# Performance work log

Measured on AMD Instinct MI355X. Metric: run time of the kernel, lower is better.

Reference implementation:

```python
import jax, jax.numpy as jnp
import numpy as np
from jax import lax

FPLANE = 256
RATIO = 0.5
C_SHIFT = int(FPLANE * RATIO)  # 128
HALF = C_SHIFT // 2            # 64


def setup_inputs() -> dict:
    key = jax.random.key(0)
    k_x, k_wl, k_bl, k_wr, k_br = jax.random.split(key, 5)
    T, C, H, W = 64, FPLANE, 56, 56
    x = jax.random.normal(k_x, (T, C, H, W), dtype=jnp.float32)
    # Conv3d(HALF -> 1, kernel (3,3,3)); original inits to zero, we use small
    # random weights so the gated path is non-trivial for kernel testing.
    scale = 1.0 / np.sqrt(HALF * 27)
    w_l = jax.random.normal(k_wl, (1, HALF, 3, 3, 3), dtype=jnp.float32) * scale
    b_l = jax.random.normal(k_bl, (1,), dtype=jnp.float32) * 0.01
    w_r = jax.random.normal(k_wr, (1, HALF, 3, 3, 3), dtype=jnp.float32) * scale
    b_r = jax.random.normal(k_br, (1,), dtype=jnp.float32) * 0.01
    return {"x": x, "w_l": w_l, "b_l": b_l, "w_r": w_r, "b_r": b_r}


def _cyclic_pad_t(x):
    # x: (1, C, T, H, W) -> pad 1 frame cyclically along T
    return jnp.concatenate([x[:, :, -1:], x, x[:, :, :1]], axis=2)


def _conv3d(x, w, b):
    # temporal padding VALID (input is cyclically pre-padded), spatial SAME
    y = lax.conv_general_dilated(
        x, w, window_strides=(1, 1, 1),
        padding=[(0, 0), (1, 1), (1, 1)],
        dimension_numbers=("NCDHW", "OIDHW", "NCDHW"))
    return y + b[None, :, None, None, None]


def reference(x, w_l, b_l, w_r, b_r):
    # x: (T, C, H, W) -> (1, C, T, H, W)
    x5 = x.transpose(1, 0, 2, 3)[None]
    x_l = x5[:, :HALF]                 # (1, half, T, H, W)
    x_r = x5[:, HALF:C_SHIFT]
    x_keep = x5[:, C_SHIFT:]

    gate_l = jnp.tanh(_conv3d(_cyclic_pad_t(x_l), w_l, b_l))  # (1,1,T,H,W)
    gate_r = jnp.tanh(_conv3d(_cyclic_pad_t(x_r), w_r, b_r))

    y_l = gate_l * x_l
    y_r = gate_r * x_r
    y_l = jnp.roll(y_l, -1, axis=2) + (x_l - y_l)
    y_r = jnp.roll(y_r, 1, axis=2) + (x_r - y_r)

    y_all = jnp.concatenate([y_l, y_r, x_keep], axis=1)  # (1, C, T, H, W)
    return y_all[0].transpose(1, 0, 2, 3)                # (T, C, H, W)
```

## Files before the change

kernel.cpp:

```cpp
#include <hip/hip_runtime.h>
#include <math.h>

#define T_DIM 64
#define C_DIM 256
#define H_DIM 56
#define W_DIM 56
#define HW    (H_DIM * W_DIM)
#define HW4   (HW / 4)
#define CHW   (C_DIM * HW)
#define THW   (T_DIM * HW)

typedef float nt_float4 __attribute__((ext_vector_type(4)));

__device__ __forceinline__ float rfl(float v) {
    return __int_as_float(__builtin_amdgcn_readfirstlane(__float_as_int(v)));
}

template<int S>
__global__ __launch_bounds__(256) void gate_kernel(
    const float* __restrict__ x,
    const float* __restrict__ w_l,
    const float* __restrict__ w_r,
    float* __restrict__ pbuf)
{
    constexpr int CPG = 64 / S;

    const int bx   = blockIdx.x;
    const int tq   = bx & 31;
    const int sg   = bx >> 5;
    const int side = sg / S;
    const int g    = sg & (S - 1);

    const int waveid = __builtin_amdgcn_readfirstlane((int)(threadIdx.x >> 6));
    const int hh = waveid & 1;
    const int t  = tq * 2 + (waveid >> 1);

    const int lane = threadIdx.x & 63;
    const int wg   = lane & 15;
    const int rg   = lane >> 4;
    const bool act = (wg < 14);
    const int w0   = act ? wg * 4 : 52;
    const int r0   = hh * 28 + rg * 7;
    const bool have_l = (wg > 0);
    const bool have_r = (wg < 13);

    const float* wtab = (side ? w_r : w_l) + g * CPG * 27;
    const int c0 = side * 64 + g * CPG;

    const int tm = (t + 63) & 63, tp = (t + 1) & 63;
    const float* tbase[3] = { x + (size_t)tm * CHW,
                              x + (size_t)t  * CHW,
                              x + (size_t)tp * CHW };

    float acc[7][4];
    #pragma unroll
    for (int j = 0; j < 7; ++j)
        #pragma unroll
        for (int k = 0; k < 4; ++k) acc[j][k] = 0.f;

    #pragma unroll 1
    for (int ci = 0; ci < CPG; ++ci) {
        float wgt[27];
        #pragma unroll
        for (int k = 0; k < 27; ++k) wgt[k] = rfl(wtab[ci * 27 + k]);

        #pragma unroll
        for (int dt = 0; dt < 3; ++dt) {
            const float* plane = tbase[dt] + (size_t)(c0 + ci) * HW;

            #pragma unroll
            for (int s9 = 0; s9 < 9; ++s9) {
                const int sr = r0 - 1 + s9;
                bool rv = true;
                int  srow = sr;
                if (s9 == 0)      { rv = (sr >= 0);     srow = rv ? sr : 0; }
                else if (s9 == 8) { rv = (sr < H_DIM);  srow = rv ? sr : (H_DIM - 1); }

                const float* row = plane + srow * W_DIM;
                float4 m  = *(const float4*)(row + w0);
                float  fl = __shfl_up(m.w, 1);
                float  fr = __shfl_down(m.x, 1);

                float f0 = have_l ? fl : 0.f;
                float f1 = m.x, f2 = m.y, f3 = m.z, f4v = m.w;
                float f5 = have_r ? fr : 0.f;
                if ((s9 == 0 || s9 == 8) && !rv) {
                    f0 = 0.f; f1 = 0.f; f2 = 0.f; f3 = 0.f; f4v = 0.f; f5 = 0.f;
                }
                float f[6] = { f0, f1, f2, f3, f4v, f5 };

                const int jlo = (s9 >= 2) ? s9 - 2 : 0;
                const int jhi = (s9 <= 6) ? s9 : 6;
                #pragma unroll
                for (int j = jlo; j <= jhi; ++j) {
                    const int dh = s9 - j;
                    const float w0t = wgt[dt * 9 + dh * 3 + 0];
                    const float w1t = wgt[dt * 9 + dh * 3 + 1];
                    const float w2t = wgt[dt * 9 + dh * 3 + 2];
                    #pragma unroll
                    for (int k = 0; k < 4; ++k)
                        acc[j][k] += w0t * f[k] + w1t * f[k + 1] + w2t * f[k + 2];
                }
            }
        }
    }

    if (act) {
        float* pp = pbuf + (size_t)sg * THW
                         + (size_t)t * HW + r0 * W_DIM + w0;
        #pragma unroll
        for (int j = 0; j < 7; ++j) {
            float4 v; v.x = acc[j][0]; v.y = acc[j][1]; v.z = acc[j][2]; v.w = acc[j][3];
            *(float4*)(pp + j * W_DIM) = v;
        }
    }
}

template<int S>
__global__ __launch_bounds__(256) void reduce_tanh_kernel(
    const float* __restrict__ pbuf,
    float* __restrict__ gbuf,
    const float* __restrict__ b_l,
    const float* __restrict__ b_r)
{
    const int i = blockIdx.x * 256 + threadIdx.x;
    const float4* p4 = (const float4*)pbuf;
    float4* g4 = (float4*)gbuf;

    float4 a = {0.f,0.f,0.f,0.f}, b = {0.f,0.f,0.f,0.f};
    #pragma unroll
    for (int g = 0; g < S; ++g) {
        float4 va = p4[(size_t)g       * (THW/4) + i];
        float4 vb = p4[(size_t)(S + g) * (THW/4) + i];
        a.x += va.x; a.y += va.y; a.z += va.z; a.w += va.w;
        b.x += vb.x; b.y += vb.y; b.z += vb.z; b.w += vb.w;
    }
    const float bl = b_l[0], br = b_r[0];
    float4 gl, gr;
    gl.x = tanhf(a.x + bl); gl.y = tanhf(a.y + bl);
    gl.z = tanhf(a.z + bl); gl.w = tanhf(a.w + bl);
    gr.x = tanhf(b.x + br); gr.y = tanhf(b.y + br);
    gr.z = tanhf(b.z + br); gr.w = tanhf(b.w + br);
    g4[i]           = gl;
    g4[(THW/4) + i] = gr;
}

__global__ __launch_bounds__(256) void combine_kernel(
    const float* __restrict__ x,
    const float* __restrict__ g,
    float* __restrict__ out)
{
    const int tid = blockIdx.x * 256 + threadIdx.x;
    const int t0  = blockIdx.y * 16;
    const int c   = tid / HW4;
    const int gb  = tid - c * HW4;

    const float4* x4 = (const float4*)x;
    float4*       o4 = (float4*)out;
    const nt_float4* xn4 = (const nt_float4*)x;
    nt_float4*       on4 = (nt_float4*)out;
    const size_t  ts = C_DIM * HW4;
    const size_t  base = tid;

    if (c >= 128) {
        #pragma unroll 4
        for (int i = 0; i < 16; ++i) {
            const size_t idx = (size_t)(t0 + i) * ts + base;
            nt_float4 v = __builtin_nontemporal_load(&xn4[idx]);
            __builtin_nontemporal_store(v, &on4[idx]);
        }
    } else if (c < 64) {
        const float4* gl4 = (const float4*)g;
        float4 xv = x4[(size_t)t0 * ts + base];
        float4 g0 = gl4[t0 * HW4 + gb];
        #pragma unroll 4
        for (int i = 0; i < 16; ++i) {
            const int t  = t0 + i;
            const int tp = (t + 1) & 63;
            float4 xn = x4[(size_t)tp * ts + base];
            float4 g1 = gl4[tp * HW4 + gb];
            nt_float4 r;
            r.x = xv.x - g0.x * xv.x + g1.x * xn.x;
            r.y = xv.y - g0.y * xv.y + g1.y * xn.y;
            r.z = xv.z - g0.z * xv.z + g1.z * xn.z;
            r.w = xv.w - g0.w * xv.w + g1.w * xn.w;
            __builtin_nontemporal_store(r, &on4[(size_t)t * ts + base]);
            xv = xn; g0 = g1;
        }
    } else {
        const float4* gr4 = (const float4*)(g + THW);
        const int tmi = (t0 + 63) & 63;
        float4 xm = x4[(size_t)tmi * ts + base];
        float4 gm = gr4[tmi * HW4 + gb];
        #pragma unroll 4
        for (int i = 0; i < 16; ++i) {
            const int t = t0 + i;
            float4 xv = x4[(size_t)t * ts + base];
            float4 g0 = gr4[t * HW4 + gb];
            nt_float4 r;
            r.x = xv.x - g0.x * xv.x + gm.x * xm.x;
            r.y = xv.y - g0.y * xv.y + gm.y * xm.y;
            r.z = xv.z - g0.z * xv.z + gm.z * xm.z;
            r.w = xv.w - g0.w * xv.w + gm.w * xm.w;
            __builtin_nontemporal_store(r, &on4[(size_t)t * ts + base]);
            xm = xv; gm = g0;
        }
    }
}

template<int S>
static void launch_all(const float* x, const float* w_l, const float* b_l,
                       const float* w_r, const float* b_r,
                       float* out, float* ws, hipStream_t stream)
{
    float* pbuf = ws;
    float* gbuf = ws + (size_t)(2 * S) * THW;
    gate_kernel<S><<<2 * S * 32, 256, 0, stream>>>(x, w_l, w_r, pbuf);
    reduce_tanh_kernel<S><<<THW / 4 / 256, 256, 0, stream>>>(pbuf, gbuf, b_l, b_r);
    combine_kernel<<<dim3(HW4 * C_DIM / 256, 4), 256, 0, stream>>>(x, gbuf, out);
}

extern "C" void kernel_launch(void* const* d_in, const int* in_sizes, int n_in,
                              void* d_out, int out_size, void* d_ws, size_t ws_size,
                              hipStream_t stream) {
    const float* x   = (const float*)d_in[0];
    const float* w_l = (const float*)d_in[1];
    const float* b_l = (const float*)d_in[2];
    const float* w_r = (const float*)d_in[3];
    const float* b_r = (const float*)d_in[4];
    float* out = (float*)d_out;
    float* ws  = (float*)d_ws;

    const size_t plane_bytes = (size_t)THW * 4;
    if (ws_size >= 34 * plane_bytes)
        launch_all<16>(x, w_l, b_l, w_r, b_r, out, ws, stream);
    else if (ws_size >= 18 * plane_bytes)
        launch_all<8>(x, w_l, b_l, w_r, b_r, out, ws, stream);
    else
        launch_all<4>(x, w_l, b_l, w_r, b_r, out, ws, stream);
}
```

Before: 113.4 us.

## Overlap passthrough channel copy with gate convolution and remap gate blocks per XCD

Moves the copy of the untouched upper 128 channels out of the combine kernel and appends it as extra blocks to the gate convolution launch, so the bandwidth-bound copy can run alongside the compute-bound convolution. The combine kernel shrinks to cover only the 128 shifted channels. Gate block indices are also remapped so that blocks sharing a channel group land on the same XCD, to improve L2 reuse of input planes. The combined launch may now contend for bandwidth with the convolution's reads and changes how blocks are scheduled.

Result: faster. 110.2 us (-2.8%).

```diff
diff --git a/kernel.cpp b/kernel.cpp
--- a/kernel.cpp
+++ b/kernel.cpp
@@ -17,17 +17,42 @@
 }
 
 template<int S>
-__global__ __launch_bounds__(256) void gate_kernel(
+__global__ __launch_bounds__(256) void gate_copy_kernel(
     const float* __restrict__ x,
     const float* __restrict__ w_l,
     const float* __restrict__ w_r,
-    float* __restrict__ pbuf)
-{
-    constexpr int CPG = 64 / S;
-
-    const int bx   = blockIdx.x;
-    const int tq   = bx & 31;
-    const int sg   = bx >> 5;
+    float* __restrict__ pbuf,
+    float* __restrict__ out)
+{
+    constexpr int CPG   = 64 / S;
+    constexpr int NGATE = 2 * S * 32;
+
+    const int p = blockIdx.x;
+
+    if (p >= NGATE) {
+        const int qq     = p - NGATE;
+        const int tchunk = qq / 392;
+        const int bx2    = qq - tchunk * 392;
+        const int tid    = 128 * HW4 + bx2 * 256 + (int)threadIdx.x;
+        const int t0     = tchunk * 16;
+
+        const nt_float4* xn4 = (const nt_float4*)x;
+        nt_float4*       on4 = (nt_float4*)out;
+        const size_t ts = C_DIM * HW4;
+
+        #pragma unroll 4
+        for (int i = 0; i < 16; ++i) {
+            const size_t idx = (size_t)(t0 + i) * ts + tid;
+            nt_float4 v = __builtin_nontemporal_load(&xn4[idx]);
+            __builtin_nontemporal_store(v, &on4[idx]);
+        }
+        return;
+    }
+
+    const int xcd = p & 7;
+    const int s   = p >> 3;
+    const int sg  = xcd * (2 * S / 8) + (s >> 5);
+    const int tq  = s & 31;
     const int side = sg / S;
     const int g    = sg & (S - 1);
 
@@ -156,20 +181,11 @@
     const int gb  = tid - c * HW4;
 
     const float4* x4 = (const float4*)x;
-    float4*       o4 = (float4*)out;
-    const nt_float4* xn4 = (const nt_float4*)x;
-    nt_float4*       on4 = (nt_float4*)out;
+    nt_float4*    on4 = (nt_float4*)out;
     const size_t  ts = C_DIM * HW4;
     const size_t  base = tid;
 
-    if (c >= 128) {
-        #pragma unroll 4
-        for (int i = 0; i < 16; ++i) {
-            const size_t idx = (size_t)(t0 + i) * ts + base;
-            nt_float4 v = __builtin_nontemporal_load(&xn4[idx]);
-            __builtin_nontemporal_store(v, &on4[idx]);
-        }
-    } else if (c < 64) {
+    if (c < 64) {
         const float4* gl4 = (const float4*)g;
         float4 xv = x4[(size_t)t0 * ts + base];
         float4 g0 = gl4[t0 * HW4 + gb];
@@ -215,9 +231,12 @@
 {
     float* pbuf = ws;
     float* gbuf = ws + (size_t)(2 * S) * THW;
-    gate_kernel<S><<<2 * S * 32, 256, 0, stream>>>(x, w_l, w_r, pbuf);
+
+    const int ngate = 2 * S * 32;
+    const int ncopy = 392 * 4;
+    gate_copy_kernel<S><<<ngate + ncopy, 256, 0, stream>>>(x, w_l, w_r, pbuf, out);
     reduce_tanh_kernel<S><<<THW / 4 / 256, 256, 0, stream>>>(pbuf, gbuf, b_l, b_r);
-    combine_kernel<<<dim3(HW4 * C_DIM / 256, 4), 256, 0, stream>>>(x, gbuf, out);
+    combine_kernel<<<dim3(392, 4), 256, 0, stream>>>(x, gbuf, out);
 }
 
 extern "C" void kernel_launch(void* const* d_in, const int* in_sizes, int n_in,
```
